# Performance work log

Hardware: AMD Instinct MI355X
Metric: run time of the kernel (lower is better)

The kernel has to match this reference:

```python
import jax, jax.numpy as jnp
import numpy as np

TEMP = 0.07
BASE_TEMP = 0.07
LOSS_WEIGHT = 0.5
BN_EPS = 1e-5


def _embed(x, w1, b1, gamma, beta, w2, b2):
    # 1x1 conv C->C  (x: [N,C,H,W], w1: [C_out,C_in])
    h = jnp.einsum('nchw,oc->nohw', x, w1) + b1[None, :, None, None]
    # BatchNorm2d in training mode: batch stats over (N,H,W), biased variance
    mean = h.mean(axis=(0, 2, 3), keepdims=True)
    var = h.var(axis=(0, 2, 3), keepdims=True)
    h = (h - mean) * jax.lax.rsqrt(var + BN_EPS)
    h = h * gamma[None, :, None, None] + beta[None, :, None, None]
    h = jax.nn.relu(h)
    h = jnp.einsum('nchw,oc->nohw', h, w2) + b2[None, :, None, None]
    # F.normalize(p=2, dim=1) with eps=1e-12
    nrm = jnp.sqrt(jnp.sum(h * h, axis=1, keepdims=True))
    return h / jnp.maximum(nrm, 1e-12)


def _contrastive(feats_, labels_):
    # feats_: [T, n_view, C]; labels_: [T]
    T, n_view, C = feats_.shape
    mask_small = (labels_[:, None] == labels_[None, :]).astype(feats_.dtype)  # [T,T]
    # torch.cat(torch.unbind(feats_, dim=1), dim=0): view-major ordering
    cf = feats_.transpose(1, 0, 2).reshape(T * n_view, C)
    logits = (cf @ cf.T) / TEMP                                   # [M,M], M=T*n_view
    logits = logits - jax.lax.stop_gradient(jnp.max(logits, axis=1, keepdims=True))
    mask = jnp.tile(mask_small, (n_view, n_view))                  # repeat(anchor_count, contrast_count)
    neg_mask = 1.0 - mask                                          # computed BEFORE diagonal removal
    M = T * n_view
    logits_mask = 1.0 - jnp.eye(M, dtype=feats_.dtype)
    mask = mask * logits_mask
    exp_logits = jnp.exp(logits)
    neg_logits = jnp.sum(exp_logits * neg_mask, axis=1, keepdims=True)
    log_prob = logits - jnp.log(exp_logits + neg_logits)
    mean_log_prob_pos = jnp.sum(mask * log_prob, axis=1) / (jnp.sum(mask, axis=1) + 1e-6)
    loss = -(TEMP / BASE_TEMP) * mean_log_prob_pos
    return jnp.mean(loss)


def setup_inputs() -> dict:
    N, C_in, H, W = 8, 512, 128, 128
    feat_dim, num_classes = 256, 19
    max_views, max_samples, ignore_label = 100, 1024, -1
    rng = np.random.RandomState(0)

    preds_S = rng.randn(N, C_in, H, W).astype(np.float32)
    # gt label map already at (H,W) => nearest interpolation is identity
    gt = rng.randint(0, num_classes, (N, H * W))
    logits_S = rng.randn(N, num_classes, H * W).astype(np.float32)
    predict = logits_S.argmax(axis=1)  # [N, H*W]

    # ---- replicate _hard_anchor_sampling on host (fixed seed) ----
    classes, total = [], 0
    for i in range(N):
        cl = [int(c) for c in np.unique(gt[i])
              if c != ignore_label and (gt[i] == c).sum() > max_views]
        classes.append(cl)
        total += len(cl)
    n_view = min(max_samples // total, max_views)

    b_idx, p_idx, y_cls = [], [], []
    for i in range(N):
        for c in classes[i]:
            hard = np.where((predict[i] == c) & (gt[i] != c))[0]
            easy = np.where((predict[i] == c) & (gt[i] == c))[0]
            nh, ne = len(hard), len(easy)
            if nh >= n_view / 2 and ne >= n_view / 2:
                kh = n_view // 2; ke = n_view - kh
            elif nh >= n_view / 2:
                ke = ne; kh = n_view - ke
            else:
                kh = nh; ke = n_view - kh
            hs = hard[rng.permutation(nh)[:kh]]
            es = easy[rng.permutation(ne)[:ke]]
            b_idx.append(i)
            p_idx.append(np.concatenate([hs, es]))
            y_cls.append(c)

    batch_idx = jnp.asarray(np.array(b_idx), dtype=jnp.int32)          # [T]
    pix_idx = jnp.asarray(np.stack(p_idx), dtype=jnp.int32)            # [T, n_view]
    y_cls = jnp.asarray(np.array(y_cls), dtype=jnp.int32)              # [T]

    def p(shape, scale, k):
        r = np.random.RandomState(k)
        return jnp.asarray((r.randn(*shape) * scale).astype(np.float32))

    return {
        'preds_S': jnp.asarray(preds_S),
        'w1': p((C_in, C_in), 0.02, 1),
        'b1': jnp.zeros((C_in,), jnp.float32),
        'gamma': jnp.ones((C_in,), jnp.float32),
        'beta': jnp.zeros((C_in,), jnp.float32),
        'w2': p((feat_dim, C_in), 0.02, 2),
        'b2': jnp.zeros((feat_dim,), jnp.float32),
        'batch_idx': batch_idx,
        'pix_idx': pix_idx,
        'y_cls': y_cls,
    }


def reference(preds_S, w1, b1, gamma, beta, w2, b2, batch_idx, pix_idx, y_cls):
    f = _embed(preds_S, w1, b1, gamma, beta, w2, b2)        # [N, C, H, W]
    N, C, H, W = f.shape
    feats = f.transpose(0, 2, 3, 1).reshape(N, H * W, C)     # [N, HW, C]
    X_ = feats[batch_idx[:, None], pix_idx]                   # [T, n_view, C]
    labels_ = y_cls.astype(f.dtype)
    return LOSS_WEIGHT * _contrastive(X_, labels_)
```

## Files before the change

### kernel.cpp

```cpp
#include <hip/hip_runtime.h>
#include <hip/hip_bf16.h>

#define C_IN   512
#define C_OUT  256
#define HW     16384
#define NIMG   8
#define PTOT   (NIMG * HW)
#define MP     1024
#define TEMP_INV (1.0f / 0.07f)
#define BN_EPS   1e-5f
#define SPB    4
#define OGRP   4
#define IGRP   4
#define BK     64

typedef float  f32x4  __attribute__((ext_vector_type(4)));
typedef short  short8 __attribute__((ext_vector_type(8)));
typedef short  short4v __attribute__((ext_vector_type(4)));

#define WS_S1   0
#define WS_G    (WS_S1 + C_IN)
#define WS_W1P  (WS_G + C_IN * C_IN)
#define WS_B1P  (WS_W1P + C_IN * C_IN)
#define WS_CF   (WS_B1P + C_IN)
#define WS_XB_F (WS_CF + MP * C_OUT)
#define WS_NEED_FAST ((size_t)WS_XB_F * 4 + (size_t)PTOT * C_IN * 2)
#define WS_PART_F (WS_XB_F + PTOT * (C_IN / 2))
#define NPART_F   (10 * 128 * 128 * 128)
#define WS_NEED_PART ((size_t)(WS_PART_F + NPART_F) * 4)

__global__ __launch_bounds__(256)
void kprep(const float* __restrict__ x, __hip_bfloat16* __restrict__ xb,
           float* __restrict__ s1) {
    int plane = blockIdx.x;
    int c = plane & (C_IN - 1);
    const float4* p = (const float4*)(x + (size_t)plane * HW);
    short4v* q = (short4v*)(xb + (size_t)plane * HW);
    float acc = 0.f;
    for (int i = threadIdx.x; i < HW / 4; i += 256) {
        float4 v = p[i];
        acc += v.x + v.y + v.z + v.w;
        union { short4v s; __hip_bfloat162 h[2]; } u;
        u.h[0] = __float22bfloat162_rn(make_float2(v.x, v.y));
        u.h[1] = __float22bfloat162_rn(make_float2(v.z, v.w));
        q[i] = u.s;
    }
    for (int off = 32; off; off >>= 1) acc += __shfl_down(acc, off, 64);
    __shared__ float red[4];
    int lane = threadIdx.x & 63, wv = threadIdx.x >> 6;
    if (lane == 0) red[wv] = acc;
    __syncthreads();
    if (threadIdx.x == 0)
        atomicAdd(&s1[c], red[0] + red[1] + red[2] + red[3]);
}

__global__ __launch_bounds__(256)
void ksum(const float* __restrict__ x, float* __restrict__ s1) {
    int plane = blockIdx.x;
    int c = plane & (C_IN - 1);
    const float4* p = (const float4*)(x + (size_t)plane * HW);
    float acc = 0.f;
    for (int i = threadIdx.x; i < HW / 4; i += 256) {
        float4 v = p[i];
        acc += v.x + v.y + v.z + v.w;
    }
    for (int off = 32; off; off >>= 1) acc += __shfl_down(acc, off, 64);
    __shared__ float red[4];
    int lane = threadIdx.x & 63, wv = threadIdx.x >> 6;
    if (lane == 0) red[wv] = acc;
    __syncthreads();
    if (threadIdx.x == 0)
        atomicAdd(&s1[c], red[0] + red[1] + red[2] + red[3]);
}

__device__ const int OI[6] = {0,0,0,1,1,2};
__device__ const int OJ[6] = {1,2,3,2,3,3};
__device__ const int TI2[10] = {0,1,2,3, 0,0,0,1,1,2};
__device__ const int TJ2[10] = {0,1,2,3, 1,2,3,2,3,3};

template<bool PART, bool DIAG>
__global__ __launch_bounds__(256, 4)
void kgram2(const __hip_bfloat16* __restrict__ xb, float* __restrict__ G,
            float* __restrict__ Gp) {
    __shared__ __hip_bfloat16 Abuf[128 * BK];
    __shared__ __hip_bfloat16 Bsto[DIAG ? 64 : 128 * BK];
    int t     = blockIdx.x;
    int chunk = blockIdx.y;
    int n   = chunk >> 4;
    int hw0 = (chunk & 15) * 1024;
    int wave = threadIdx.x >> 6;
    int lane = threadIdx.x & 63;
    int wi = wave >> 1, wj = wave & 1;
    int IT, JT;
    if (DIAG) { IT = t * 128; JT = IT; }
    else      { IT = OI[t] * 128; JT = OJ[t] * 128; }

    const __hip_bfloat16* gA = xb + ((size_t)n * C_IN + IT) * HW + hw0;
    const __hip_bfloat16* gB = xb + ((size_t)n * C_IN + JT) * HW + hw0;

    int rrel = lane >> 3;
    int slot = lane & 7;

    f32x4 acc[4][4];
#pragma unroll
    for (int i = 0; i < 4; ++i)
#pragma unroll
        for (int j = 0; j < 4; ++j) acc[i][j] = {0.f, 0.f, 0.f, 0.f};

    int m  = lane & 15;
    int kq = lane >> 4;

#pragma unroll 1
    for (int s = 0; s < 16; ++s) {
        int kk = s * BK;
#pragma unroll
        for (int i_ = 0; i_ < 4; ++i_) {
            int row = wave * 32 + i_ * 8 + rrel;
            int g   = slot ^ (row & 7);
            __builtin_amdgcn_global_load_lds(
                (const __attribute__((address_space(1))) void*)
                    (gA + (size_t)row * HW + kk + g * 8),
                (__attribute__((address_space(3))) void*)
                    (&Abuf[(wave * 32 + i_ * 8) * BK]),
                16, 0, 0);
            if (!DIAG)
                __builtin_amdgcn_global_load_lds(
                    (const __attribute__((address_space(1))) void*)
                        (gB + (size_t)row * HW + kk + g * 8),
                    (__attribute__((address_space(3))) void*)
                        (&Bsto[(wave * 32 + i_ * 8) * BK]),
                    16, 0, 0);
        }
        __syncthreads();
#pragma unroll
        for (int h = 0; h < 2; ++h) {
            short8 af[4], bf[4];
#pragma unroll
            for (int t_ = 0; t_ < 4; ++t_) {
                int ra = wi * 64 + t_ * 16 + m;
                int qa = (h * 4 + kq) ^ (ra & 7);
                af[t_] = *(const short8*)&Abuf[ra * BK + qa * 8];
                int rb = wj * 64 + t_ * 16 + m;
                int qb = (h * 4 + kq) ^ (rb & 7);
                bf[t_] = DIAG ? *(const short8*)&Abuf[rb * BK + qb * 8]
                              : *(const short8*)&Bsto[rb * BK + qb * 8];
            }
#pragma unroll
            for (int i_ = 0; i_ < 4; ++i_)
#pragma unroll
                for (int j_ = 0; j_ < 4; ++j_)
                    acc[i_][j_] = __builtin_amdgcn_mfma_f32_16x16x32_bf16(
                        af[i_], bf[j_], acc[i_][j_], 0, 0, 0);
        }
        __syncthreads();
    }

    int r0 = (lane >> 4) * 4;
    int cc = lane & 15;
    if (PART) {
        int tileid = DIAG ? t : (4 + t);
        float* P = Gp + ((size_t)tileid * 128 + chunk) * (128 * 128);
#pragma unroll
        for (int i = 0; i < 4; ++i)
#pragma unroll
            for (int j = 0; j < 4; ++j)
#pragma unroll
                for (int r = 0; r < 4; ++r)
                    P[(wi * 64 + i * 16 + r0 + r) * 128 + (wj * 64 + j * 16 + cc)]
                        = acc[i][j][r];
    } else {
#pragma unroll
        for (int i = 0; i < 4; ++i)
#pragma unroll
            for (int j = 0; j < 4; ++j)
#pragma unroll
                for (int r = 0; r < 4; ++r)
                    atomicAdd(&G[(size_t)(IT + wi * 64 + i * 16 + r0 + r) * C_IN
                                 + (JT + wj * 64 + j * 16 + cc)],
                              acc[i][j][r]);
    }
}

__global__ __launch_bounds__(256)
void kgacc(const float* __restrict__ Gp, float* __restrict__ G) {
    int tile = blockIdx.x >> 4;
    int seg  = blockIdx.x & 15;
    int IT = TI2[tile] * 128, JT = TJ2[tile] * 128;
    int e0 = seg * 1024 + threadIdx.x * 4;
    const float* base = Gp + (size_t)tile * 128 * (128 * 128) + e0;
    f32x4 a0 = {0,0,0,0}, a1 = {0,0,0,0}, a2 = {0,0,0,0}, a3 = {0,0,0,0};
    for (int ch = 0; ch < 128; ch += 4) {
        a0 += *(const f32x4*)(base + (size_t)(ch + 0) * (128 * 128));
        a1 += *(const f32x4*)(base + (size_t)(ch + 1) * (128 * 128));
        a2 += *(const f32x4*)(base + (size_t)(ch + 2) * (128 * 128));
        a3 += *(const f32x4*)(base + (size_t)(ch + 3) * (128 * 128));
    }
    f32x4 s = (a0 + a1) + (a2 + a3);
    int r = e0 >> 7, c = e0 & 127;
    *(f32x4*)(&G[(size_t)(IT + r) * C_IN + JT + c]) = s;
    if (IT != JT) {
#pragma unroll
        for (int k = 0; k < 4; ++k)
            G[(size_t)(JT + c + k) * C_IN + IT + r] = s[k];
    }
}

__global__ __launch_bounds__(256)
void kmirror(float* __restrict__ G) {
    int i = blockIdx.x;
    for (int j = threadIdx.x; j < C_IN; j += 256) {
        if ((i >> 7) > (j >> 7))
            G[(size_t)i * C_IN + j] = G[(size_t)j * C_IN + i];
    }
}

__device__ inline short8 load_frag_f32(const float* p) {
    float4 a = *(const float4*)p;
    float4 b = *(const float4*)(p + 4);
    union { short8 s; __hip_bfloat162 h[4]; } u;
    u.h[0] = __float22bfloat162_rn(make_float2(a.x, a.y));
    u.h[1] = __float22bfloat162_rn(make_float2(a.z, a.w));
    u.h[2] = __float22bfloat162_rn(make_float2(b.x, b.y));
    u.h[3] = __float22bfloat162_rn(make_float2(b.z, b.w));
    return u.s;
}

__global__ __launch_bounds__(256)
void kgram_f32(const float* __restrict__ x, float* __restrict__ G) {
    int bz  = blockIdx.z;
    int n   = bz >> 2;
    int hw0 = (bz & 3) * 4096;
    int wave = threadIdx.x >> 6;
    int lane = threadIdx.x & 63;
    int wi = wave >> 1, wj = wave & 1;
    int I0 = blockIdx.x * 128 + wi * 64;
    int J0 = blockIdx.y * 128 + wj * 64;
    int m    = lane & 15;
    int koff = (lane >> 4) * 8;

    const float* baseA[4];
    const float* baseB[4];
#pragma unroll
    for (int t = 0; t < 4; ++t) {
        baseA[t] = x + ((size_t)n * C_IN + (I0 + t * 16 + m)) * HW + hw0 + koff;
        baseB[t] = x + ((size_t)n * C_IN + (J0 + t * 16 + m)) * HW + hw0 + koff;
    }

    f32x4 acc[4][4];
#pragma unroll
    for (int i = 0; i < 4; ++i)
#pragma unroll
        for (int j = 0; j < 4; ++j) acc[i][j] = {0.f, 0.f, 0.f, 0.f};

    for (int kk = 0; kk < 4096; kk += 32) {
        short8 afr[4], bfr[4];
#pragma unroll
        for (int t = 0; t < 4; ++t) {
            afr[t] = load_frag_f32(baseA[t] + kk);
            bfr[t] = load_frag_f32(baseB[t] + kk);
        }
#pragma unroll
        for (int i = 0; i < 4; ++i)
#pragma unroll
            for (int j = 0; j < 4; ++j)
                acc[i][j] = __builtin_amdgcn_mfma_f32_16x16x32_bf16(
                    afr[i], bfr[j], acc[i][j], 0, 0, 0);
    }

    int r0 = (lane >> 4) * 4;
    int cc = lane & 15;
#pragma unroll
    for (int i = 0; i < 4; ++i)
#pragma unroll
        for (int j = 0; j < 4; ++j)
#pragma unroll
            for (int r = 0; r < 4; ++r)
                atomicAdd(&G[(size_t)(I0 + i * 16 + r0 + r) * C_IN + (J0 + j * 16 + cc)],
                          acc[i][j][r]);
}

__global__ __launch_bounds__(256)
void kstats(const float* __restrict__ w1, const float* __restrict__ b1,
            const float* __restrict__ gamma, const float* __restrict__ beta,
            const float* __restrict__ s1, const float* __restrict__ G,
            float* __restrict__ w1p, float* __restrict__ b1p) {
    int o0 = blockIdx.x * OGRP;
    int tid = threadIdx.x;
    __shared__ float wr[OGRP][C_IN];
    __shared__ float redd[4][OGRP];
    __shared__ float redq[4][OGRP];
    __shared__ float alpha_s[OGRP];

    for (int idx = tid; idx < OGRP * C_IN; idx += 256) {
        int og = idx >> 9, c = idx & (C_IN - 1);
        wr[og][c] = w1[(size_t)(o0 + og) * C_IN + c];
    }
    __syncthreads();

    float dot1[OGRP], quad[OGRP];
#pragma unroll
    for (int og = 0; og < OGRP; ++og) { dot1[og] = 0.f; quad[og] = 0.f; }

    for (int c = tid; c < C_IN; c += 256) {
        const float* gr = G + (size_t)c * C_IN;
        float s1c = s1[c];
        float inner[OGRP];
#pragma unroll
        for (int og = 0; og < OGRP; ++og) inner[og] = 0.f;
        for (int d = 0; d < C_IN; d += 4) {
            float4 gv = *(const float4*)(gr + d);
#pragma unroll
            for (int og = 0; og < OGRP; ++og) {
                float4 wv = *(const float4*)(&wr[og][d]);
                inner[og] += gv.x * wv.x + gv.y * wv.y + gv.z * wv.z + gv.w * wv.w;
            }
        }
#pragma unroll
        for (int og = 0; og < OGRP; ++og) {
            float wc = wr[og][c];
            quad[og] += inner[og] * wc;
            dot1[og] += s1c * wc;
        }
    }
#pragma unroll
    for (int og = 0; og < OGRP; ++og) {
        for (int off = 32; off; off >>= 1) {
            dot1[og] += __shfl_down(dot1[og], off, 64);
            quad[og] += __shfl_down(quad[og], off, 64);
        }
    }
    int lane = tid & 63, wv = tid >> 6;
    if (lane == 0) {
#pragma unroll
        for (int og = 0; og < OGRP; ++og) { redd[wv][og] = dot1[og]; redq[wv][og] = quad[og]; }
    }
    __syncthreads();
    if (tid < OGRP) {
        int og = tid;
        float d1 = redd[0][og] + redd[1][og] + redd[2][og] + redd[3][og];
        float q  = redq[0][og] + redq[1][og] + redq[2][og] + redq[3][og];
        float b  = b1[o0 + og];
        float mean = d1 / (float)PTOT + b;
        float eh2  = (q + 2.f * b * d1) / (float)PTOT + b * b;
        float var  = eh2 - mean * mean;
        float al   = gamma[o0 + og] * rsqrtf(var + BN_EPS);
        alpha_s[og] = al;
        b1p[o0 + og] = beta[o0 + og] + al * (b - mean);
    }
    __syncthreads();
    for (int idx = tid; idx < OGRP * C_IN; idx += 256) {
        int og = idx >> 9, c = idx & (C_IN - 1);
        w1p[(size_t)(o0 + og) * C_IN + c] = alpha_s[og] * wr[og][c];
    }
}

__global__ __launch_bounds__(256)
void kfeat(const float* __restrict__ x, const float* __restrict__ w1p,
           const float* __restrict__ b1p, const float* __restrict__ w2,
           const float* __restrict__ b2, const int* __restrict__ batch_idx,
           const int* __restrict__ pix_idx, float* __restrict__ cf,
           int M, int T, int n_view) {
    __shared__ float xcol[SPB][C_IN];
    __shared__ float h1[SPB][C_IN];
    __shared__ float fl[SPB][C_OUT];
    int tid = threadIdx.x;
    int m0 = blockIdx.x * SPB;

    for (int idx = tid; idx < SPB * C_IN; idx += 256) {
        int s = idx >> 9, c = idx & (C_IN - 1);
        int mm = m0 + s;
        float v = 0.f;
        if (mm < M) {
            int t = mm % T, vv = mm / T;
            int n = batch_idx[t];
            int pix = pix_idx[t * n_view + vv];
            v = x[((size_t)n * C_IN + c) * HW + pix];
        }
        xcol[s][c] = v;
    }
    __syncthreads();

    for (int o = tid; o < C_IN; o += 256) {
        float acc[SPB];
        float bb = b1p[o];
#pragma unroll
        for (int s = 0; s < SPB; ++s) acc[s] = bb;
        const float* wrp = w1p + (size_t)o * C_IN;
        for (int c = 0; c < C_IN; c += 4) {
            float4 w = *(const float4*)(wrp + c);
#pragma unroll
            for (int s = 0; s < SPB; ++s) {
                float4 xv = *(const float4*)(&xcol[s][c]);
                acc[s] += w.x * xv.x + w.y * xv.y + w.z * xv.z + w.w * xv.w;
            }
        }
#pragma unroll
        for (int s = 0; s < SPB; ++s) h1[s][o] = fmaxf(acc[s], 0.f);
    }
    __syncthreads();

    {
        int j = tid;
        float acc[SPB];
        float bb = b2[j];
#pragma unroll
        for (int s = 0; s < SPB; ++s) acc[s] = bb;
        const float* wrp = w2 + (size_t)j * C_IN;
        for (int o = 0; o < C_IN; o += 4) {
            float4 w = *(const float4*)(wrp + o);
#pragma unroll
            for (int s = 0; s < SPB; ++s) {
                float4 hv = *(const float4*)(&h1[s][o]);
                acc[s] += w.x * hv.x + w.y * hv.y + w.z * hv.z + w.w * hv.w;
            }
        }
#pragma unroll
        for (int s = 0; s < SPB; ++s) fl[s][j] = acc[s];
    }
    __syncthreads();

    int wv = tid >> 6, lane = tid & 63;
    {
        float sq = 0.f;
#pragma unroll
        for (int k = 0; k < 4; ++k) { float v = fl[wv][lane + 64 * k]; sq += v * v; }
        for (int off = 32; off; off >>= 1) sq += __shfl_down(sq, off, 64);
        float nrm = __shfl(sq, 0, 64);
        float rinv = 1.f / fmaxf(sqrtf(nrm), 1e-12f);
        int mm = m0 + wv;
        if (mm < M) {
#pragma unroll
            for (int k = 0; k < 4; ++k)
                cf[(size_t)mm * C_OUT + lane + 64 * k] = fl[wv][lane + 64 * k] * rinv;
        }
    }
}

__global__ __launch_bounds__(256)
void kloss(const float* __restrict__ cf, const int* __restrict__ y_cls,
           float* __restrict__ out, int M, int T) {
    int i0 = blockIdx.x * IGRP;
    int tid = threadIdx.x;
    __shared__ float ci[IGRP][C_OUT];
    __shared__ float row[IGRP][MP];
    __shared__ int   lbl[MP];
    __shared__ float redl[IGRP];
    int lane = tid & 63, wv = tid >> 6;

    for (int idx = tid; idx < IGRP * C_OUT; idx += 256) {
        int g = idx >> 8, c = idx & (C_OUT - 1);
        int ii = i0 + g;
        ci[g][c] = (ii < M) ? cf[(size_t)ii * C_OUT + c] : 0.f;
    }
    for (int j = tid; j < M; j += 256) lbl[j] = y_cls[j % T];
    __syncthreads();

    for (int j = tid; j < M; j += 256) {
        const float* cj = cf + (size_t)j * C_OUT;
        float acc[IGRP];
#pragma unroll
        for (int g = 0; g < IGRP; ++g) acc[g] = 0.f;
        for (int c = 0; c < C_OUT; c += 4) {
            float4 v = *(const float4*)(cj + c);
#pragma unroll
            for (int g = 0; g < IGRP; ++g) {
                float4 cv = *(const float4*)(&ci[g][c]);
                acc[g] += cv.x * v.x + cv.y * v.y + cv.z * v.z + cv.w * v.w;
            }
        }
#pragma unroll
        for (int g = 0; g < IGRP; ++g) row[g][j] = acc[g] * TEMP_INV;
    }
    __syncthreads();

    for (int g = wv; g < IGRP; g += 4) {
        int i = i0 + g;
        if (i < M) {
            int lbl_i = lbl[i];
            const float* r = row[g];

            float mx = -1e30f;
            for (int j = lane; j < M; j += 64) mx = fmaxf(mx, r[j]);
            for (int off = 32; off; off >>= 1) mx = fmaxf(mx, __shfl_down(mx, off, 64));
            mx = __shfl(mx, 0, 64);

            float neg = 0.f;
            for (int j = lane; j < M; j += 64)
                if (lbl[j] != lbl_i) neg += expf(r[j] - mx);
            for (int off = 32; off; off >>= 1) neg += __shfl_down(neg, off, 64);
            neg = __shfl(neg, 0, 64);

            float pos = 0.f; int cnt = 0;
            for (int j = lane; j < M; j += 64) {
                if (lbl[j] == lbl_i && j != i) {
                    float l = r[j] - mx;
                    pos += l - logf(expf(l) + neg);
                    cnt++;
                }
            }
            for (int off = 32; off; off >>= 1) {
                pos += __shfl_down(pos, off, 64);
                cnt += __shfl_down(cnt, off, 64);
            }
            if (lane == 0) redl[g] = -pos / ((float)cnt + 1e-6f);
        } else if (lane == 0) redl[g] = 0.f;
    }
    __syncthreads();
    if (tid == 0) {
        float s = 0.f;
        for (int g = 0; g < IGRP; ++g) s += redl[g];
        atomicAdd(out, s * (0.5f / (float)M));
    }
}

extern "C" void kernel_launch(void* const* d_in, const int* in_sizes, int n_in,
                              void* d_out, int out_size, void* d_ws, size_t ws_size,
                              hipStream_t stream) {
    const float* x     = (const float*)d_in[0];
    const float* w1    = (const float*)d_in[1];
    const float* b1    = (const float*)d_in[2];
    const float* gamma = (const float*)d_in[3];
    const float* beta  = (const float*)d_in[4];
    const float* w2    = (const float*)d_in[5];
    const float* b2    = (const float*)d_in[6];
    const int* batch_idx = (const int*)d_in[7];
    const int* pix_idx   = (const int*)d_in[8];
    const int* y_cls     = (const int*)d_in[9];

    int T = in_sizes[7];
    int M = in_sizes[8];
    int n_view = M / T;

    float* ws  = (float*)d_ws;
    float* s1  = ws + WS_S1;
    float* G   = ws + WS_G;
    float* w1p = ws + WS_W1P;
    float* b1p = ws + WS_B1P;
    float* cf  = ws + WS_CF;
    __hip_bfloat16* xb = (__hip_bfloat16*)(ws + WS_XB_F);
    float* Gpart = ws + WS_PART_F;

    hipMemsetAsync(d_out, 0, sizeof(float), stream);

    if (ws_size >= WS_NEED_PART) {
        hipMemsetAsync(s1, 0, (size_t)C_IN * sizeof(float), stream);
        kprep<<<NIMG * C_IN, 256, 0, stream>>>(x, xb, s1);
        kgram2<true, true ><<<dim3(4, 128), 256, 0, stream>>>(xb, G, Gpart);
        kgram2<true, false><<<dim3(6, 128), 256, 0, stream>>>(xb, G, Gpart);
        kgacc<<<160, 256, 0, stream>>>(Gpart, G);
    } else if (ws_size >= WS_NEED_FAST) {
        hipMemsetAsync(s1, 0, (size_t)(C_IN + C_IN * C_IN) * sizeof(float), stream);
        kprep<<<NIMG * C_IN, 256, 0, stream>>>(x, xb, s1);
        kgram2<false, true ><<<dim3(4, 128), 256, 0, stream>>>(xb, G, nullptr);
        kgram2<false, false><<<dim3(6, 128), 256, 0, stream>>>(xb, G, nullptr);
        kmirror<<<C_IN, 256, 0, stream>>>(G);
    } else {
        hipMemsetAsync(s1, 0, (size_t)(C_IN + C_IN * C_IN) * sizeof(float), stream);
        ksum<<<NIMG * C_IN, 256, 0, stream>>>(x, s1);
        kgram_f32<<<dim3(4, 4, 32), 256, 0, stream>>>(x, G);
    }
    kstats<<<C_IN / OGRP, 256, 0, stream>>>(w1, b1, gamma, beta, s1, G, w1p, b1p);
    kfeat<<<(M + SPB - 1) / SPB, 256, 0, stream>>>(x, w1p, b1p, w2, b2,
                                                   batch_idx, pix_idx, cf, M, T, n_view);
    kloss<<<(M + IGRP - 1) / IGRP, 256, 0, stream>>>(cf, y_cls, (float*)d_out, M, T);
}
```

Before: 672.5 us.

## Merge Gram launches, double K chunk size, drop memsets via per-plane sums

The two Gram kernels (diagonal and off-diagonal tiles) become a single launch over all 10 tiles, with the diagonal case chosen at runtime. Each block now covers a 2048-wide K chunk, which halves the number of partial tiles that the reduction kernel must read. Per-plane channel sums are written directly instead of accumulated with atomics, so the s1 and output memsets go away and the output is zeroed inside kprep. The cost is a larger LDS buffer, since diagonal blocks also allocate the B buffer, and a lower occupancy bound of 3 blocks per CU.

```diff
diff --git a/kernel.cpp b/kernel.cpp
--- a/kernel.cpp
+++ b/kernel.cpp
@@ -13,27 +13,29 @@
 #define OGRP   4
 #define IGRP   4
 #define BK     64
+#define KCH    2048
+#define NCHUNK (PTOT / KCH)
 
 typedef float  f32x4  __attribute__((ext_vector_type(4)));
 typedef short  short8 __attribute__((ext_vector_type(8)));
 typedef short  short4v __attribute__((ext_vector_type(4)));
 
 #define WS_S1   0
-#define WS_G    (WS_S1 + C_IN)
+#define WS_G    (WS_S1 + NIMG * C_IN)
 #define WS_W1P  (WS_G + C_IN * C_IN)
 #define WS_B1P  (WS_W1P + C_IN * C_IN)
 #define WS_CF   (WS_B1P + C_IN)
 #define WS_XB_F (WS_CF + MP * C_OUT)
 #define WS_NEED_FAST ((size_t)WS_XB_F * 4 + (size_t)PTOT * C_IN * 2)
 #define WS_PART_F (WS_XB_F + PTOT * (C_IN / 2))
-#define NPART_F   (10 * 128 * 128 * 128)
+#define NPART_F   (10 * NCHUNK * 128 * 128)
 #define WS_NEED_PART ((size_t)(WS_PART_F + NPART_F) * 4)
 
 __global__ __launch_bounds__(256)
 void kprep(const float* __restrict__ x, __hip_bfloat16* __restrict__ xb,
-           float* __restrict__ s1) {
+           float* __restrict__ s1p, float* __restrict__ out) {
     int plane = blockIdx.x;
-    int c = plane & (C_IN - 1);
+    if (plane == 0 && threadIdx.x == 0) *out = 0.f;
     const float4* p = (const float4*)(x + (size_t)plane * HW);
     short4v* q = (short4v*)(xb + (size_t)plane * HW);
     float acc = 0.f;
@@ -51,13 +53,13 @@
     if (lane == 0) red[wv] = acc;
     __syncthreads();
     if (threadIdx.x == 0)
-        atomicAdd(&s1[c], red[0] + red[1] + red[2] + red[3]);
-}
-
-__global__ __launch_bounds__(256)
-void ksum(const float* __restrict__ x, float* __restrict__ s1) {
+        s1p[plane] = red[0] + red[1] + red[2] + red[3];
+}
+
+__global__ __launch_bounds__(256)
+void ksum(const float* __restrict__ x, float* __restrict__ s1p, float* __restrict__ out) {
     int plane = blockIdx.x;
-    int c = plane & (C_IN - 1);
+    if (plane == 0 && threadIdx.x == 0) *out = 0.f;
     const float4* p = (const float4*)(x + (size_t)plane * HW);
     float acc = 0.f;
     for (int i = threadIdx.x; i < HW / 4; i += 256) {
@@ -70,30 +72,28 @@
     if (lane == 0) red[wv] = acc;
     __syncthreads();
     if (threadIdx.x == 0)
-        atomicAdd(&s1[c], red[0] + red[1] + red[2] + red[3]);
-}
-
-__device__ const int OI[6] = {0,0,0,1,1,2};
-__device__ const int OJ[6] = {1,2,3,2,3,3};
+        s1p[plane] = red[0] + red[1] + red[2] + red[3];
+}
+
 __device__ const int TI2[10] = {0,1,2,3, 0,0,0,1,1,2};
 __device__ const int TJ2[10] = {0,1,2,3, 1,2,3,2,3,3};
 
-template<bool PART, bool DIAG>
-__global__ __launch_bounds__(256, 4)
+template<bool PART>
+__global__ __launch_bounds__(256, 3)
 void kgram2(const __hip_bfloat16* __restrict__ xb, float* __restrict__ G,
             float* __restrict__ Gp) {
-    __shared__ __hip_bfloat16 Abuf[128 * BK];
-    __shared__ __hip_bfloat16 Bsto[DIAG ? 64 : 128 * BK];
-    int t     = blockIdx.x;
+    __shared__ __hip_bfloat16 buf[2][128 * BK];
+    int tile  = blockIdx.x;
+    int IT = TI2[tile] * 128;
+    int JT = TJ2[tile] * 128;
+    bool diag = (IT == JT);
+    int bsel = diag ? 0 : 1;
     int chunk = blockIdx.y;
-    int n   = chunk >> 4;
-    int hw0 = (chunk & 15) * 1024;
+    int n   = chunk >> 3;
+    int hw0 = (chunk & 7) * KCH;
     int wave = threadIdx.x >> 6;
     int lane = threadIdx.x & 63;
     int wi = wave >> 1, wj = wave & 1;
-    int IT, JT;
-    if (DIAG) { IT = t * 128; JT = IT; }
-    else      { IT = OI[t] * 128; JT = OJ[t] * 128; }
 
     const __hip_bfloat16* gA = xb + ((size_t)n * C_IN + IT) * HW + hw0;
     const __hip_bfloat16* gB = xb + ((size_t)n * C_IN + JT) * HW + hw0;
@@ -111,7 +111,7 @@
     int kq = lane >> 4;
 
 #pragma unroll 1
-    for (int s = 0; s < 16; ++s) {
+    for (int s = 0; s < KCH / BK; ++s) {
         int kk = s * BK;
 #pragma unroll
         for (int i_ = 0; i_ < 4; ++i_) {
@@ -121,14 +121,14 @@
                 (const __attribute__((address_space(1))) void*)
                     (gA + (size_t)row * HW + kk + g * 8),
                 (__attribute__((address_space(3))) void*)
-                    (&Abuf[(wave * 32 + i_ * 8) * BK]),
+                    (&buf[0][(wave * 32 + i_ * 8) * BK]),
                 16, 0, 0);
-            if (!DIAG)
+            if (!diag)
                 __builtin_amdgcn_global_load_lds(
                     (const __attribute__((address_space(1))) void*)
                         (gB + (size_t)row * HW + kk + g * 8),
                     (__attribute__((address_space(3))) void*)
-                        (&Bsto[(wave * 32 + i_ * 8) * BK]),
+                        (&buf[1][(wave * 32 + i_ * 8) * BK]),
                     16, 0, 0);
         }
         __syncthreads();
@@ -139,11 +139,10 @@
             for (int t_ = 0; t_ < 4; ++t_) {
                 int ra = wi * 64 + t_ * 16 + m;
                 int qa = (h * 4 + kq) ^ (ra & 7);
-                af[t_] = *(const short8*)&Abuf[ra * BK + qa * 8];
+                af[t_] = *(const short8*)&buf[0][ra * BK + qa * 8];
                 int rb = wj * 64 + t_ * 16 + m;
                 int qb = (h * 4 + kq) ^ (rb & 7);
-                bf[t_] = DIAG ? *(const short8*)&Abuf[rb * BK + qb * 8]
-                              : *(const short8*)&Bsto[rb * BK + qb * 8];
+                bf[t_] = *(const short8*)&buf[bsel][rb * BK + qb * 8];
             }
 #pragma unroll
             for (int i_ = 0; i_ < 4; ++i_)
@@ -158,8 +157,7 @@
     int r0 = (lane >> 4) * 4;
     int cc = lane & 15;
     if (PART) {
-        int tileid = DIAG ? t : (4 + t);
-        float* P = Gp + ((size_t)tileid * 128 + chunk) * (128 * 128);
+        float* P = Gp + ((size_t)tile * NCHUNK + chunk) * (128 * 128);
 #pragma unroll
         for (int i = 0; i < 4; ++i)
 #pragma unroll
@@ -187,9 +185,9 @@
     int seg  = blockIdx.x & 15;
     int IT = TI2[tile] * 128, JT = TJ2[tile] * 128;
     int e0 = seg * 1024 + threadIdx.x * 4;
-    const float* base = Gp + (size_t)tile * 128 * (128 * 128) + e0;
+    const float* base = Gp + (size_t)tile * NCHUNK * (128 * 128) + e0;
     f32x4 a0 = {0,0,0,0}, a1 = {0,0,0,0}, a2 = {0,0,0,0}, a3 = {0,0,0,0};
-    for (int ch = 0; ch < 128; ch += 4) {
+    for (int ch = 0; ch < NCHUNK; ch += 4) {
         a0 += *(const f32x4*)(base + (size_t)(ch + 0) * (128 * 128));
         a1 += *(const f32x4*)(base + (size_t)(ch + 1) * (128 * 128));
         a2 += *(const f32x4*)(base + (size_t)(ch + 2) * (128 * 128));
@@ -282,7 +280,7 @@
 __global__ __launch_bounds__(256)
 void kstats(const float* __restrict__ w1, const float* __restrict__ b1,
             const float* __restrict__ gamma, const float* __restrict__ beta,
-            const float* __restrict__ s1, const float* __restrict__ G,
+            const float* __restrict__ s1p, const float* __restrict__ G,
             float* __restrict__ w1p, float* __restrict__ b1p) {
     int o0 = blockIdx.x * OGRP;
     int tid = threadIdx.x;
@@ -303,7 +301,9 @@
 
     for (int c = tid; c < C_IN; c += 256) {
         const float* gr = G + (size_t)c * C_IN;
-        float s1c = s1[c];
+        float s1c = 0.f;
+#pragma unroll
+        for (int nn = 0; nn < NIMG; ++nn) s1c += s1p[nn * C_IN + c];
         float inner[OGRP];
 #pragma unroll
         for (int og = 0; og < OGRP; ++og) inner[og] = 0.f;
@@ -532,7 +532,7 @@
     int n_view = M / T;
 
     float* ws  = (float*)d_ws;
-    float* s1  = ws + WS_S1;
+    float* s1p = ws + WS_S1;
     float* G   = ws + WS_G;
     float* w1p = ws + WS_W1P;
     float* b1p = ws + WS_B1P;
@@ -540,26 +540,21 @@
     __hip_bfloat16* xb = (__hip_bfloat16*)(ws + WS_XB_F);
     float* Gpart = ws + WS_PART_F;
 
-    hipMemsetAsync(d_out, 0, sizeof(float), stream);
-
     if (ws_size >= WS_NEED_PART) {
-        hipMemsetAsync(s1, 0, (size_t)C_IN * sizeof(float), stream);
-        kprep<<<NIMG * C_IN, 256, 0, stream>>>(x, xb, s1);
-        kgram2<true, true ><<<dim3(4, 128), 256, 0, stream>>>(xb, G, Gpart);
-        kgram2<true, false><<<dim3(6, 128), 256, 0, stream>>>(xb, G, Gpart);
+        kprep<<<NIMG * C_IN, 256, 0, stream>>>(x, xb, s1p, (float*)d_out);
+        kgram2<true><<<dim3(10, NCHUNK), 256, 0, stream>>>(xb, G, Gpart);
         kgacc<<<160, 256, 0, stream>>>(Gpart, G);
     } else if (ws_size >= WS_NEED_FAST) {
-        hipMemsetAsync(s1, 0, (size_t)(C_IN + C_IN * C_IN) * sizeof(float), stream);
-        kprep<<<NIMG * C_IN, 256, 0, stream>>>(x, xb, s1);
-        kgram2<false, true ><<<dim3(4, 128), 256, 0, stream>>>(xb, G, nullptr);
-        kgram2<false, false><<<dim3(6, 128), 256, 0, stream>>>(xb, G, nullptr);
+        hipMemsetAsync(G, 0, (size_t)(C_IN * C_IN) * sizeof(float), stream);
+        kprep<<<NIMG * C_IN, 256, 0, stream>>>(x, xb, s1p, (float*)d_out);
+        kgram2<false><<<dim3(10, NCHUNK), 256, 0, stream>>>(xb, G, nullptr);
         kmirror<<<C_IN, 256, 0, stream>>>(G);
     } else {
-        hipMemsetAsync(s1, 0, (size_t)(C_IN + C_IN * C_IN) * sizeof(float), stream);
-        ksum<<<NIMG * C_IN, 256, 0, stream>>>(x, s1);
+        hipMemsetAsync(G, 0, (size_t)(C_IN * C_IN) * sizeof(float), stream);
+        ksum<<<NIMG * C_IN, 256, 0, stream>>>(x, s1p, (float*)d_out);
         kgram_f32<<<dim3(4, 4, 32), 256, 0, stream>>>(x, G);
     }
-    kstats<<<C_IN / OGRP, 256, 0, stream>>>(w1, b1, gamma, beta, s1, G, w1p, b1p);
+    kstats<<<C_IN / OGRP, 256, 0, stream>>>(w1, b1, gamma, beta, s1p, G, w1p, b1p);
     kfeat<<<(M + SPB - 1) / SPB, 256, 0, stream>>>(x, w1p, b1p, w2, b2,
                                                    batch_idx, pix_idx, cf, M, T, n_view);
     kloss<<<(M + IGRP - 1) / IGRP, 256, 0, stream>>>(cf, y_cls, (float*)d_out, M, T);
```

Result: faster. 629.3 us (-6.4%).
